# Optimization experiments

Hardware: AMD Instinct MI355X
Metric: run time of the kernel (lower is better)

Reference implementation:

```python
import jax, jax.numpy as jnp
import numpy as np

HEADS = 16
DIM = 1024
SCALE = DIM ** (-0.5)  # scale_with_head=False


def setup_inputs() -> dict:
    key = jax.random.key(0)
    k1, k2, k3, k4, k5 = jax.random.split(key, 5)
    B, N = 8, 1024
    x = jax.random.normal(k1, (B, N, DIM), dtype=jnp.float32)
    mask = jax.random.bernoulli(k2, 0.9, (B, N - 1))  # bool [B, N-1]
    Wqkv = jax.random.normal(k3, (3 * DIM, DIM), dtype=jnp.float32) * 0.02
    Wout = jax.random.normal(k4, (DIM, DIM), dtype=jnp.float32) * 0.02
    bout = jax.random.normal(k5, (DIM,), dtype=jnp.float32) * 0.02
    return {"x": x, "mask": mask, "Wqkv": Wqkv, "Wout": Wout, "bout": bout}


def reference(x, mask, Wqkv, Wout, bout):
    b, n, dim = x.shape
    h = HEADS
    d = dim // h
    qkv = x @ Wqkv.T  # [b, n, 3*dim]
    q, k, v = jnp.split(qkv, 3, axis=-1)
    # b n (h d) -> b h n d
    def to_heads(t):
        return t.reshape(b, n, h, d).transpose(0, 2, 1, 3)
    q, k, v = to_heads(q), to_heads(k), to_heads(v)
    dots = jnp.einsum('bhid,bhjd->bhij', q, k) * SCALE  # [b, h, n, n]
    # F.pad(mask.flatten(1), (1,0), value=True) -> prepend always-true token
    m = jnp.pad(mask, ((0, 0), (1, 0)), constant_values=True)  # [b, n]
    pair = m[:, None, None, :] & m[:, None, :, None]  # [b, 1, n, n]
    mask_value = -jnp.finfo(dots.dtype).max
    dots = jnp.where(pair, dots, mask_value)
    attn = jax.nn.softmax(dots, axis=-1)
    out = jnp.einsum('bhij,bhjd->bhid', attn, v)  # [b, h, n, d]
    out = out.transpose(0, 2, 1, 3).reshape(b, n, dim)  # b h n d -> b n (h d)
    out = out @ Wout.T + bout  # to_out (dropout=0 -> identity)
    return out
```

## Files before the change

### kernel.cpp

```cpp
#include <hip/hip_runtime.h>
#include <hip/hip_bf16.h>
#include <stdint.h>

typedef __hip_bfloat16 bf16;
typedef unsigned short u16;
typedef __attribute__((ext_vector_type(8))) short short8;
typedef __attribute__((ext_vector_type(4))) float f32x4;
typedef __attribute__((ext_vector_type(16))) float f32x16;
typedef __attribute__((ext_vector_type(4))) int int4v;

#define BATCH 8
#define SEQ   1024
#define DIM   1024
#define NHEAD 16
#define HD    64
#define SCALE 0.03125f
#define C2    0.04508422f

static __device__ __forceinline__ f32x4 mfma_bf16(short8 a, short8 b, f32x4 c) {
    return __builtin_amdgcn_mfma_f32_16x16x32_bf16(a, b, c, 0, 0, 0);
}
static __device__ __forceinline__ f32x16 mfma32(short8 a, short8 b, f32x16 c) {
    return __builtin_amdgcn_mfma_f32_32x32x16_bf16(a, b, c, 0, 0, 0);
}
static __device__ __forceinline__ unsigned cvt_pk_bf16(float lo, float hi) {
    unsigned r;
    asm("v_cvt_pk_bf16_f32 %0, %1, %2" : "=v"(r) : "v"(lo), "v"(hi));
    return r;
}
static __device__ __forceinline__ void gload16(const u16* g, u16* l) {
    __builtin_amdgcn_global_load_lds(
        (const __attribute__((address_space(1))) void*)g,
        (__attribute__((address_space(3))) void*)l, 16, 0, 0);
}

static __device__ __forceinline__ void conv_seg(const void* src, u16* dst,
                                                int total, int bloc, int bcnt,
                                                bool f32in)
{
    for (int i = bloc * 256 + (int)threadIdx.x; i < total; i += bcnt * 256) {
        if (f32in) {
            const float4 a = ((const float4*)src)[2 * i];
            const float4 b = ((const float4*)src)[2 * i + 1];
            short8 o;
            o[0] = (short)__builtin_bit_cast(u16, __float2bfloat16(a.x));
            o[1] = (short)__builtin_bit_cast(u16, __float2bfloat16(a.y));
            o[2] = (short)__builtin_bit_cast(u16, __float2bfloat16(a.z));
            o[3] = (short)__builtin_bit_cast(u16, __float2bfloat16(a.w));
            o[4] = (short)__builtin_bit_cast(u16, __float2bfloat16(b.x));
            o[5] = (short)__builtin_bit_cast(u16, __float2bfloat16(b.y));
            o[6] = (short)__builtin_bit_cast(u16, __float2bfloat16(b.z));
            o[7] = (short)__builtin_bit_cast(u16, __float2bfloat16(b.w));
            ((short8*)dst)[i] = o;
        } else {
            ((short8*)dst)[i] = ((const short8*)src)[i];
        }
    }
}

__global__ __launch_bounds__(256)
void prep_all(const void* __restrict__ x, const void* __restrict__ mask,
              const void* __restrict__ wq, const void* __restrict__ wo,
              const void* __restrict__ bo,
              u16* __restrict__ xb, u16* __restrict__ wqb,
              u16* __restrict__ wob, u16* __restrict__ bob,
              unsigned long long* __restrict__ mask64)
{
    __shared__ int s_cnt[2];
    if (threadIdx.x == 0) { s_cnt[0] = 0; s_cnt[1] = 0; }
    __syncthreads();
    {
        const uint32_t wx = ((const uint32_t*)x)[threadIdx.x];
        const int e = (int)((wx >> 7) & 0xFFu);
        if (e >= 96 && e <= 159) atomicAdd(&s_cnt[0], 1);
        const uint32_t wm = ((const uint32_t*)mask)[threadIdx.x];
        if (wm > 1u) atomicAdd(&s_cnt[1], 1);
    }
    __syncthreads();
    const bool f32in = (s_cnt[0] < 192);
    const bool mbyte = (s_cnt[1] > 0);

    const int bid = blockIdx.x;
    if (bid < 2048)       conv_seg(x,  xb,  1048576, bid,        2048, f32in);
    else if (bid < 2816)  conv_seg(wq, wqb, 393216,  bid - 2048,  768, f32in);
    else if (bid < 3072)  conv_seg(wo, wob, 131072,  bid - 2816,  256, f32in);
    else if (bid == 3072) conv_seg(bo, bob, 128,     0,             1, f32in);
    else {
        const int b = bid - 3073;
#pragma unroll
        for (int c = 0; c < 4; ++c) {
            const int i = c * 256 + (int)threadIdx.x;
            int v;
            if (i == 0) v = 1;
            else if (mbyte) v = (int)((const uint8_t*)mask)[b * (SEQ - 1) + i - 1];
            else            v = ((const int*)mask)[b * (SEQ - 1) + i - 1];
            v = v ? 1 : 0;
            const unsigned long long bal = __ballot(v);
            if ((i & 63) == 0) mask64[b * 16 + (i >> 6)] = bal;
        }
    }
}

template<int EPI>
__global__ __launch_bounds__(256)
void gemm_bt(const u16* __restrict__ A, const u16* __restrict__ Bm,
             bf16* __restrict__ o0, bf16* __restrict__ o1, bf16* __restrict__ o2,
             float* __restrict__ fo, const u16* __restrict__ bias)
{
    constexpr int K   = 1024;
    constexpr int NT  = K / 64;
    constexpr int BUF = 256 * 64;
    __shared__ u16 lds[2 * BUF];

    const int tid  = threadIdx.x;
    const int lane = tid & 63;
    const int w    = tid >> 6;
    const int wr   = w >> 1, wc = w & 1;
    const int l15  = lane & 15, l4 = lane >> 4;

    const long atile = (long)blockIdx.x * 128;
    const long btile = (long)blockIdx.y * 128;

    const int rl  = lane >> 3;
    const int gs8 = ((lane & 7) ^ rl) * 8;
    const u16* gp[8];
#pragma unroll
    for (int j = 0; j < 8; ++j) {
        const int g = 8 * w + j;
        const int r = g * 8 + rl;
        gp[j] = (r < 128) ? A  + (atile + r) * (long)K + gs8
                          : Bm + (btile + (r - 128)) * (long)K + gs8;
    }

    const int lx  = l4 ^ (l15 & 3);
    const int b2  = (l15 >> 2) & 1;
    const int sl0 = (b2 * 4 + lx) * 8;
    const int sl1 = (((1 ^ b2) * 4) + lx) * 8;
    const int arow = wr * 64 + l15;
    const int brow = 128 + wc * 64 + l15;

    f32x4 acc[4][4];
    const f32x4 fz = {0.f, 0.f, 0.f, 0.f};
#pragma unroll
    for (int i = 0; i < 4; ++i)
#pragma unroll
        for (int j = 0; j < 4; ++j) acc[i][j] = fz;

#define STG(bufo, kt, j) gload16(gp[j] + (size_t)(kt) * 64, \
                                 &lds[(bufo) + (8 * w + (j)) * 512])

#pragma unroll
    for (int j = 0; j < 8; ++j) STG(0, 0, j);
    asm volatile("s_waitcnt vmcnt(0)" ::: "memory");
    __builtin_amdgcn_s_barrier();
    __builtin_amdgcn_sched_barrier(0);

    int cur = 0;
#pragma unroll 1
    for (int kt = 0; kt < NT; ++kt) {
        const int co = cur * BUF;
        const int no = (cur ^ 1) * BUF;
        short8 bfr[2][4], af0, af1;

#pragma unroll
        for (int nt = 0; nt < 4; ++nt) {
            bfr[0][nt] = *(const short8*)&lds[co + (brow + nt * 16) * 64 + sl0];
            bfr[1][nt] = *(const short8*)&lds[co + (brow + nt * 16) * 64 + sl1];
        }
        af0 = *(const short8*)&lds[co + arow * 64 + sl0];
        af1 = *(const short8*)&lds[co + arow * 64 + sl1];
        if (kt + 1 < NT) {
            STG(no, kt + 1, 0); STG(no, kt + 1, 1);
            STG(no, kt + 1, 2); STG(no, kt + 1, 3);
        }
        asm volatile("s_waitcnt lgkmcnt(0)" ::: "memory");
        __builtin_amdgcn_sched_barrier(0);
        __builtin_amdgcn_s_setprio(1);
#pragma unroll
        for (int nt = 0; nt < 4; ++nt) {
            acc[0][nt] = mfma_bf16(af0, bfr[0][nt], acc[0][nt]);
            acc[0][nt] = mfma_bf16(af1, bfr[1][nt], acc[0][nt]);
        }
        __builtin_amdgcn_s_setprio(0);

#pragma unroll
        for (int mt = 1; mt < 4; ++mt) {
            af0 = *(const short8*)&lds[co + (arow + mt * 16) * 64 + sl0];
            af1 = *(const short8*)&lds[co + (arow + mt * 16) * 64 + sl1];
            if (mt == 1 && kt + 1 < NT) {
                STG(no, kt + 1, 4); STG(no, kt + 1, 5);
                STG(no, kt + 1, 6); STG(no, kt + 1, 7);
            }
            asm volatile("s_waitcnt lgkmcnt(0)" ::: "memory");
            __builtin_amdgcn_sched_barrier(0);
            __builtin_amdgcn_s_setprio(1);
#pragma unroll
            for (int nt = 0; nt < 4; ++nt) {
                acc[mt][nt] = mfma_bf16(af0, bfr[0][nt], acc[mt][nt]);
                acc[mt][nt] = mfma_bf16(af1, bfr[1][nt], acc[mt][nt]);
            }
            __builtin_amdgcn_s_setprio(0);
        }

        asm volatile("s_waitcnt vmcnt(0)" ::: "memory");
        __builtin_amdgcn_s_barrier();
        __builtin_amdgcn_sched_barrier(0);
        cur ^= 1;
    }
#undef STG

    const long ci0 = atile + wr * 64;
    const int  cj0 = (int)btile + wc * 64;
#pragma unroll
    for (int mt = 0; mt < 4; ++mt) {
#pragma unroll
        for (int nt = 0; nt < 4; ++nt) {
            const int j = cj0 + nt * 16 + l15;
#pragma unroll
            for (int r = 0; r < 4; ++r) {
                const long i = ci0 + mt * 16 + l4 * 4 + r;
                float vv = acc[mt][nt][r];
                if (EPI == 0) {
                    const int which = j >> 10;
                    const int h     = (j >> 6) & 15;
                    const int dd    = j & 63;
                    const long b    = i >> 10;
                    const long n    = i & 1023;
                    const long bhh  = b * NHEAD + h;
                    if (which == 0)
                        o0[(bhh * SEQ + n) * HD + dd] = __float2bfloat16(vv * C2);
                    else if (which == 1)
                        o1[(bhh * SEQ + n) * HD + dd] = __float2bfloat16(vv);
                    else
                        o2[(bhh * HD + dd) * SEQ + n] = __float2bfloat16(vv);
                } else {
                    const u16 bw = bias[j];
                    vv += __bfloat162float(__builtin_bit_cast(bf16, bw));
                    fo[i * DIM + j] = vv;
                }
            }
        }
    }
}

__global__ __launch_bounds__(256)
void attn_fwd(const bf16* __restrict__ q, const bf16* __restrict__ k,
              const bf16* __restrict__ vt_g,
              const unsigned long long* __restrict__ mask64,
              bf16* __restrict__ o)
{
    __shared__ u16 kl[2][64 * 72];
    __shared__ u16 vl[2][64 * 72];

    const int tid  = threadIdx.x;
    const int lane = tid & 63;
    const int w    = tid >> 6;
    const int l31  = lane & 31;
    const int hi   = lane >> 5;
    const int bh   = blockIdx.x >> 3;
    const int qt   = blockIdx.x & 7;
    const int b    = bh >> 4;
    const int h    = bh & 15;

    const long base  = (long)bh * SEQ * HD;
    const long vbase = (long)bh * HD * SEQ;

    const int qrow = qt * 128 + w * 32 + l31;
    const int mi   = (int)((mask64[b * 16 + (qrow >> 6)] >> (qrow & 63)) & 1ull);

    short8 qf[4];
#pragma unroll
    for (int s4 = 0; s4 < 4; ++s4)
        qf[s4] = *(const short8*)(q + base + (long)qrow * HD + s4 * 16 + hi * 8);
    if (!mi) {
#pragma unroll
        for (int s4 = 0; s4 < 4; ++s4)
            qf[s4] = __builtin_bit_cast(short8, (int4v){0, 0, 0, 0});
    }

    f32x16 oacc0, oacc1, oaccS, zc;
#pragma unroll
    for (int i = 0; i < 16; ++i)
        { oacc0[i] = 0.f; oacc1[i] = 0.f; oaccS[i] = 0.f; zc[i] = 0.f; }

    const u16 NEGW = __builtin_bit_cast(u16, __float2bfloat16(-1e30f));
    const short8 vfB = __builtin_bit_cast(short8,
        (int4v){(hi == 0 && mi) ? 0x3F80 : 0, 0, 0, 0});
    const short8 vfS = __builtin_bit_cast(short8,
        (int4v){0x3F803F80, 0x3F803F80, 0x3F803F80, 0x3F803F80});

    const int sr = tid >> 2, sc = tid & 3;
    short8 rk0 = *(const short8*)(k + base + (long)sr * HD + sc * 8);
    short8 rk1 = *(const short8*)(k + base + (long)sr * HD + 32 + sc * 8);
    short8 rv0 = *(const short8*)(vt_g + vbase + (long)sr * SEQ + sc * 8);
    short8 rv1 = *(const short8*)(vt_g + vbase + (long)sr * SEQ + 32 + sc * 8);
    *(short8*)&kl[0][sr * 72 + sc * 8]      = rk0;
    *(short8*)&kl[0][sr * 72 + 32 + sc * 8] = rk1;
    *(short8*)&vl[0][sr * 72 + sc * 8]      = rv0;
    *(short8*)&vl[0][sr * 72 + 32 + sc * 8] = rv1;
    __syncthreads();

#pragma unroll 1
    for (int t = 0; t < 16; ++t) {
        const int cb = t & 1;
        if (t < 15) {
            const long kn = base + (long)((t + 1) * 64 + sr) * HD;
            rk0 = *(const short8*)(k + kn + sc * 8);
            rk1 = *(const short8*)(k + kn + 32 + sc * 8);
            const long vn = vbase + (long)sr * SEQ + (t + 1) * 64;
            rv0 = *(const short8*)(vt_g + vn + sc * 8);
            rv1 = *(const short8*)(vt_g + vn + 32 + sc * 8);
        }

        const unsigned long long mk = mask64[b * 16 + t];
        const unsigned bit0 = (unsigned)(mk >> l31) & 1u;
        const unsigned bit1 = (unsigned)(mk >> (32 + l31)) & 1u;
        const short8 paB0 = __builtin_bit_cast(short8,
            (int4v){(hi == 0 && !bit0) ? (int)(unsigned)NEGW : 0, 0, 0, 0});
        const short8 paB1 = __builtin_bit_cast(short8,
            (int4v){(hi == 0 && !bit1) ? (int)(unsigned)NEGW : 0, 0, 0, 0});

        f32x16 s0 = mfma32(paB0, vfB, zc);
        f32x16 s1 = mfma32(paB1, vfB, zc);
#pragma unroll
        for (int s4 = 0; s4 < 4; ++s4) {
            const short8 kf0 = *(const short8*)&kl[cb][l31 * 72 + s4 * 16 + hi * 8];
            const short8 kf1 = *(const short8*)&kl[cb][(32 + l31) * 72 + s4 * 16 + hi * 8];
            s0 = mfma32(kf0, qf[s4], s0);
            s1 = mfma32(kf1, qf[s4], s1);
        }

#pragma unroll
        for (int kt = 0; kt < 2; ++kt) {
            const f32x16* sp = kt ? &s1 : &s0;
#pragma unroll
            for (int ks = 0; ks < 2; ++ks) {
                float p[8];
#pragma unroll
                for (int e = 0; e < 8; ++e)
                    p[e] = __builtin_amdgcn_exp2f((*sp)[8 * ks + e]);
                unsigned w0 = cvt_pk_bf16(p[0], p[1]);
                unsigned w1 = cvt_pk_bf16(p[2], p[3]);
                unsigned w2 = cvt_pk_bf16(p[4], p[5]);
                unsigned w3 = cvt_pk_bf16(p[6], p[7]);
                asm volatile("v_permlane32_swap_b32 %0, %1" : "+v"(w0), "+v"(w2));
                asm volatile("v_permlane32_swap_b32 %0, %1" : "+v"(w1), "+v"(w3));
                const short8 pa = __builtin_bit_cast(short8,
                    (int4v){(int)w0, (int)w1, (int)w2, (int)w3});
                const int koff = kt * 32 + ks * 16 + hi * 8;
                const short8 vf0 = *(const short8*)&vl[cb][l31 * 72 + koff];
                const short8 vf1 = *(const short8*)&vl[cb][(32 + l31) * 72 + koff];
                oacc0 = mfma32(pa, vf0, oacc0);
                oacc1 = mfma32(pa, vf1, oacc1);
                oaccS = mfma32(pa, vfS, oaccS);
            }
        }

        if (t < 15) {
            *(short8*)&kl[cb ^ 1][sr * 72 + sc * 8]      = rk0;
            *(short8*)&kl[cb ^ 1][sr * 72 + 32 + sc * 8] = rk1;
            *(short8*)&vl[cb ^ 1][sr * 72 + sc * 8]      = rv0;
            *(short8*)&vl[cb ^ 1][sr * 72 + 32 + sc * 8] = rv1;
        }
        __syncthreads();
    }

#pragma unroll
    for (int g = 0; g < 4; ++g)
#pragma unroll
        for (int j = 0; j < 4; ++j) {
            const int idx = g * 4 + j;
            const float lv = __builtin_amdgcn_rcpf(oaccS[idx]);
            const int qg = qt * 128 + w * 32 + g * 8 + j + 4 * hi;
            const long oaddr = ((long)(b * SEQ + qg)) * DIM + h * HD;
            o[oaddr + l31]      = __float2bfloat16(oacc0[idx] * lv);
            o[oaddr + 32 + l31] = __float2bfloat16(oacc1[idx] * lv);
        }
}

extern "C" void kernel_launch(void* const* d_in, const int* in_sizes, int n_in,
                              void* d_out, int out_size, void* d_ws, size_t ws_size,
                              hipStream_t stream)
{
    (void)in_sizes; (void)n_in; (void)out_size; (void)ws_size;
    const void* x    = d_in[0];
    const void* mask = d_in[1];
    const void* Wqkv = d_in[2];
    const void* Wout = d_in[3];
    const void* bout = d_in[4];
    float* out = (float*)d_out;

    const size_t nX    = (size_t)BATCH * SEQ * DIM;
    const size_t nWqkv = (size_t)3 * DIM * DIM;
    const size_t nWout = (size_t)DIM * DIM;
    const size_t nBout = DIM;
    const size_t per   = (size_t)BATCH * NHEAD * SEQ * HD;

    char* wp = (char*)d_ws;
    u16* xb    = (u16*)wp;                      wp += nX * 2;
    u16* Wqkvb = (u16*)wp;                      wp += nWqkv * 2;
    u16* Woutb = (u16*)wp;                      wp += nWout * 2;
    u16* boutb = (u16*)wp;                      wp += nBout * 2;
    unsigned long long* m64 = (unsigned long long*)wp; wp += BATCH * 16 * 8;
    u16* qb    = (u16*)wp;                      wp += per * 2;
    u16* kb    = (u16*)wp;                      wp += per * 2;
    u16* vb    = (u16*)wp;                      wp += per * 2;

    prep_all<<<3081, 256, 0, stream>>>(x, mask, Wqkv, Wout, bout,
                                       xb, Wqkvb, Woutb, boutb, m64);

    gemm_bt<0><<<dim3(64, 24), 256, 0, stream>>>(xb, Wqkvb,
        (bf16*)qb, (bf16*)kb, (bf16*)vb, nullptr, nullptr);
    bf16* ab = (bf16*)xb;
    attn_fwd<<<dim3(BATCH * NHEAD * 8), 256, 0, stream>>>(
        (const bf16*)qb, (const bf16*)kb, (const bf16*)vb, m64, ab);
    gemm_bt<1><<<dim3(64, 8), 256, 0, stream>>>((const u16*)ab, Woutb,
        nullptr, nullptr, nullptr, out, boutb);
}
```

Before: 159.8 us.

## Widen GEMM block tile to 128x256 and stream B fragments with prefetch

```diff
diff --git a/kernel.cpp b/kernel.cpp
--- a/kernel.cpp
+++ b/kernel.cpp
@@ -102,14 +102,14 @@
 }
 
 template<int EPI>
-__global__ __launch_bounds__(256)
+__global__ __launch_bounds__(256, 1)
 void gemm_bt(const u16* __restrict__ A, const u16* __restrict__ Bm,
              bf16* __restrict__ o0, bf16* __restrict__ o1, bf16* __restrict__ o2,
              float* __restrict__ fo, const u16* __restrict__ bias)
 {
     constexpr int K   = 1024;
     constexpr int NT  = K / 64;
-    constexpr int BUF = 256 * 64;
+    constexpr int BUF = 384 * 64;
     __shared__ u16 lds[2 * BUF];
 
     const int tid  = threadIdx.x;
@@ -119,14 +119,14 @@
     const int l15  = lane & 15, l4 = lane >> 4;
 
     const long atile = (long)blockIdx.x * 128;
-    const long btile = (long)blockIdx.y * 128;
+    const long btile = (long)blockIdx.y * 256;
 
     const int rl  = lane >> 3;
     const int gs8 = ((lane & 7) ^ rl) * 8;
-    const u16* gp[8];
-#pragma unroll
-    for (int j = 0; j < 8; ++j) {
-        const int g = 8 * w + j;
+    const u16* gp[12];
+#pragma unroll
+    for (int j = 0; j < 12; ++j) {
+        const int g = 12 * w + j;
         const int r = g * 8 + rl;
         gp[j] = (r < 128) ? A  + (atile + r) * (long)K + gs8
                           : Bm + (btile + (r - 128)) * (long)K + gs8;
@@ -136,21 +136,21 @@
     const int b2  = (l15 >> 2) & 1;
     const int sl0 = (b2 * 4 + lx) * 8;
     const int sl1 = (((1 ^ b2) * 4) + lx) * 8;
-    const int arow = wr * 64 + l15;
-    const int brow = 128 + wc * 64 + l15;
-
-    f32x4 acc[4][4];
+    const int ar  = wr * 64 + l15;
+    const int br  = 128 + wc * 128 + l15;
+
+    f32x4 acc[4][8];
     const f32x4 fz = {0.f, 0.f, 0.f, 0.f};
 #pragma unroll
     for (int i = 0; i < 4; ++i)
 #pragma unroll
-        for (int j = 0; j < 4; ++j) acc[i][j] = fz;
+        for (int j = 0; j < 8; ++j) acc[i][j] = fz;
 
 #define STG(bufo, kt, j) gload16(gp[j] + (size_t)(kt) * 64, \
-                                 &lds[(bufo) + (8 * w + (j)) * 512])
-
-#pragma unroll
-    for (int j = 0; j < 8; ++j) STG(0, 0, j);
+                                 &lds[(bufo) + (12 * w + (j)) * 512])
+
+#pragma unroll
+    for (int j = 0; j < 12; ++j) STG(0, 0, j);
     asm volatile("s_waitcnt vmcnt(0)" ::: "memory");
     __builtin_amdgcn_s_barrier();
     __builtin_amdgcn_sched_barrier(0);
@@ -160,46 +160,34 @@
     for (int kt = 0; kt < NT; ++kt) {
         const int co = cur * BUF;
         const int no = (cur ^ 1) * BUF;
-        short8 bfr[2][4], af0, af1;
-
-#pragma unroll
-        for (int nt = 0; nt < 4; ++nt) {
-            bfr[0][nt] = *(const short8*)&lds[co + (brow + nt * 16) * 64 + sl0];
-            bfr[1][nt] = *(const short8*)&lds[co + (brow + nt * 16) * 64 + sl1];
-        }
-        af0 = *(const short8*)&lds[co + arow * 64 + sl0];
-        af1 = *(const short8*)&lds[co + arow * 64 + sl1];
-        if (kt + 1 < NT) {
-            STG(no, kt + 1, 0); STG(no, kt + 1, 1);
-            STG(no, kt + 1, 2); STG(no, kt + 1, 3);
-        }
-        asm volatile("s_waitcnt lgkmcnt(0)" ::: "memory");
-        __builtin_amdgcn_sched_barrier(0);
-        __builtin_amdgcn_s_setprio(1);
-#pragma unroll
-        for (int nt = 0; nt < 4; ++nt) {
-            acc[0][nt] = mfma_bf16(af0, bfr[0][nt], acc[0][nt]);
-            acc[0][nt] = mfma_bf16(af1, bfr[1][nt], acc[0][nt]);
-        }
-        __builtin_amdgcn_s_setprio(0);
-
-#pragma unroll
-        for (int mt = 1; mt < 4; ++mt) {
-            af0 = *(const short8*)&lds[co + (arow + mt * 16) * 64 + sl0];
-            af1 = *(const short8*)&lds[co + (arow + mt * 16) * 64 + sl1];
-            if (mt == 1 && kt + 1 < NT) {
-                STG(no, kt + 1, 4); STG(no, kt + 1, 5);
-                STG(no, kt + 1, 6); STG(no, kt + 1, 7);
+        const bool st = (kt + 1 < NT);
+
+        short8 af[4][2];
+#pragma unroll
+        for (int mt = 0; mt < 4; ++mt) {
+            af[mt][0] = *(const short8*)&lds[co + (ar + mt * 16) * 64 + sl0];
+            af[mt][1] = *(const short8*)&lds[co + (ar + mt * 16) * 64 + sl1];
+        }
+        short8 bc0 = *(const short8*)&lds[co + br * 64 + sl0];
+        short8 bc1 = *(const short8*)&lds[co + br * 64 + sl1];
+
+#pragma unroll
+        for (int p = 0; p < 8; ++p) {
+            short8 bn0, bn1;
+            if (p < 7) {
+                bn0 = *(const short8*)&lds[co + (br + (p + 1) * 16) * 64 + sl0];
+                bn1 = *(const short8*)&lds[co + (br + (p + 1) * 16) * 64 + sl1];
             }
-            asm volatile("s_waitcnt lgkmcnt(0)" ::: "memory");
+            if (p < 6 && st) { STG(no, kt + 1, 2 * p); STG(no, kt + 1, 2 * p + 1); }
+            if (p < 7) asm volatile("s_waitcnt lgkmcnt(2)" ::: "memory");
+            else       asm volatile("s_waitcnt lgkmcnt(0)" ::: "memory");
             __builtin_amdgcn_sched_barrier(0);
-            __builtin_amdgcn_s_setprio(1);
-#pragma unroll
-            for (int nt = 0; nt < 4; ++nt) {
-                acc[mt][nt] = mfma_bf16(af0, bfr[0][nt], acc[mt][nt]);
-                acc[mt][nt] = mfma_bf16(af1, bfr[1][nt], acc[mt][nt]);
-            }
-            __builtin_amdgcn_s_setprio(0);
+#pragma unroll
+            for (int kk = 0; kk < 2; ++kk)
+#pragma unroll
+                for (int mt = 0; mt < 4; ++mt)
+                    acc[mt][p] = mfma_bf16(af[mt][kk], kk ? bc1 : bc0, acc[mt][p]);
+            if (p < 7) { bc0 = bn0; bc1 = bn1; }
         }
 
         asm volatile("s_waitcnt vmcnt(0)" ::: "memory");
@@ -210,11 +198,11 @@
 #undef STG
 
     const long ci0 = atile + wr * 64;
-    const int  cj0 = (int)btile + wc * 64;
+    const int  cj0 = (int)btile + wc * 128;
 #pragma unroll
     for (int mt = 0; mt < 4; ++mt) {
 #pragma unroll
-        for (int nt = 0; nt < 4; ++nt) {
+        for (int nt = 0; nt < 8; ++nt) {
             const int j = cj0 + nt * 16 + l15;
 #pragma unroll
             for (int r = 0; r < 4; ++r) {
@@ -409,11 +397,11 @@
     prep_all<<<3081, 256, 0, stream>>>(x, mask, Wqkv, Wout, bout,
                                        xb, Wqkvb, Woutb, boutb, m64);
 
-    gemm_bt<0><<<dim3(64, 24), 256, 0, stream>>>(xb, Wqkvb,
+    gemm_bt<0><<<dim3(64, 12), 256, 0, stream>>>(xb, Wqkvb,
         (bf16*)qb, (bf16*)kb, (bf16*)vb, nullptr, nullptr);
     bf16* ab = (bf16*)xb;
     attn_fwd<<<dim3(BATCH * NHEAD * 8), 256, 0, stream>>>(
         (const bf16*)qb, (const bf16*)kb, (const bf16*)vb, m64, ab);
-    gemm_bt<1><<<dim3(64, 8), 256, 0, stream>>>((const u16*)ab, Woutb,
+    gemm_bt<1><<<dim3(64, 4), 256, 0, stream>>>((const u16*)ab, Woutb,
         nullptr, nullptr, nullptr, out, boutb);
 }
```

Result: slower. 176.8 us (+10.6%).

## Enlarge GEMM tile to 256x128 with 512 threads and triple-buffered LDS prefetch

Applied to the files above, without the earlier changes.

```diff
diff --git a/kernel.cpp b/kernel.cpp
--- a/kernel.cpp
+++ b/kernel.cpp
@@ -102,15 +102,15 @@
 }
 
 template<int EPI>
-__global__ __launch_bounds__(256)
+__global__ __launch_bounds__(512, 1)
 void gemm_bt(const u16* __restrict__ A, const u16* __restrict__ Bm,
              bf16* __restrict__ o0, bf16* __restrict__ o1, bf16* __restrict__ o2,
              float* __restrict__ fo, const u16* __restrict__ bias)
 {
     constexpr int K   = 1024;
     constexpr int NT  = K / 64;
-    constexpr int BUF = 256 * 64;
-    __shared__ u16 lds[2 * BUF];
+    constexpr int BUF = 384 * 64;
+    __shared__ u16 lds[3 * BUF];
 
     const int tid  = threadIdx.x;
     const int lane = tid & 63;
@@ -118,26 +118,26 @@
     const int wr   = w >> 1, wc = w & 1;
     const int l15  = lane & 15, l4 = lane >> 4;
 
-    const long atile = (long)blockIdx.x * 128;
+    const long atile = (long)blockIdx.x * 256;
     const long btile = (long)blockIdx.y * 128;
 
     const int rl  = lane >> 3;
     const int gs8 = ((lane & 7) ^ rl) * 8;
-    const u16* gp[8];
-#pragma unroll
-    for (int j = 0; j < 8; ++j) {
-        const int g = 8 * w + j;
+    const u16* gp[6];
+#pragma unroll
+    for (int j = 0; j < 6; ++j) {
+        const int g = 6 * w + j;
         const int r = g * 8 + rl;
-        gp[j] = (r < 128) ? A  + (atile + r) * (long)K + gs8
-                          : Bm + (btile + (r - 128)) * (long)K + gs8;
+        gp[j] = (r < 256) ? A  + (atile + r) * (long)K + gs8
+                          : Bm + (btile + (r - 256)) * (long)K + gs8;
     }
 
     const int lx  = l4 ^ (l15 & 3);
     const int b2  = (l15 >> 2) & 1;
     const int sl0 = (b2 * 4 + lx) * 8;
     const int sl1 = (((1 ^ b2) * 4) + lx) * 8;
-    const int arow = wr * 64 + l15;
-    const int brow = 128 + wc * 64 + l15;
+    const int ar  = wr * 64 + l15;
+    const int br  = 256 + wc * 64 + l15;
 
     f32x4 acc[4][4];
     const f32x4 fz = {0.f, 0.f, 0.f, 0.f};
@@ -147,32 +147,31 @@
         for (int j = 0; j < 4; ++j) acc[i][j] = fz;
 
 #define STG(bufo, kt, j) gload16(gp[j] + (size_t)(kt) * 64, \
-                                 &lds[(bufo) + (8 * w + (j)) * 512])
-
-#pragma unroll
-    for (int j = 0; j < 8; ++j) STG(0, 0, j);
-    asm volatile("s_waitcnt vmcnt(0)" ::: "memory");
+                                 &lds[(bufo) + (6 * w + (j)) * 512])
+
+#pragma unroll
+    for (int j = 0; j < 6; ++j) STG(0, 0, j);
+#pragma unroll
+    for (int j = 0; j < 6; ++j) STG(BUF, 1, j);
+    asm volatile("s_waitcnt vmcnt(6)" ::: "memory");
     __builtin_amdgcn_s_barrier();
     __builtin_amdgcn_sched_barrier(0);
 
-    int cur = 0;
 #pragma unroll 1
     for (int kt = 0; kt < NT; ++kt) {
-        const int co = cur * BUF;
-        const int no = (cur ^ 1) * BUF;
+        const int co = (kt % 3) * BUF;
+        const int so = ((kt + 2) % 3) * BUF;
+        const bool st = (kt + 2 < NT);
         short8 bfr[2][4], af0, af1;
 
 #pragma unroll
         for (int nt = 0; nt < 4; ++nt) {
-            bfr[0][nt] = *(const short8*)&lds[co + (brow + nt * 16) * 64 + sl0];
-            bfr[1][nt] = *(const short8*)&lds[co + (brow + nt * 16) * 64 + sl1];
-        }
-        af0 = *(const short8*)&lds[co + arow * 64 + sl0];
-        af1 = *(const short8*)&lds[co + arow * 64 + sl1];
-        if (kt + 1 < NT) {
-            STG(no, kt + 1, 0); STG(no, kt + 1, 1);
-            STG(no, kt + 1, 2); STG(no, kt + 1, 3);
-        }
+            bfr[0][nt] = *(const short8*)&lds[co + (br + nt * 16) * 64 + sl0];
+            bfr[1][nt] = *(const short8*)&lds[co + (br + nt * 16) * 64 + sl1];
+        }
+        af0 = *(const short8*)&lds[co + ar * 64 + sl0];
+        af1 = *(const short8*)&lds[co + ar * 64 + sl1];
+        if (st) { STG(so, kt + 2, 0); STG(so, kt + 2, 1); }
         asm volatile("s_waitcnt lgkmcnt(0)" ::: "memory");
         __builtin_amdgcn_sched_barrier(0);
         __builtin_amdgcn_s_setprio(1);
@@ -185,12 +184,9 @@
 
 #pragma unroll
         for (int mt = 1; mt < 4; ++mt) {
-            af0 = *(const short8*)&lds[co + (arow + mt * 16) * 64 + sl0];
-            af1 = *(const short8*)&lds[co + (arow + mt * 16) * 64 + sl1];
-            if (mt == 1 && kt + 1 < NT) {
-                STG(no, kt + 1, 4); STG(no, kt + 1, 5);
-                STG(no, kt + 1, 6); STG(no, kt + 1, 7);
-            }
+            af0 = *(const short8*)&lds[co + (ar + mt * 16) * 64 + sl0];
+            af1 = *(const short8*)&lds[co + (ar + mt * 16) * 64 + sl1];
+            if (st && mt < 3) { STG(so, kt + 2, 2 * mt); STG(so, kt + 2, 2 * mt + 1); }
             asm volatile("s_waitcnt lgkmcnt(0)" ::: "memory");
             __builtin_amdgcn_sched_barrier(0);
             __builtin_amdgcn_s_setprio(1);
@@ -202,10 +198,10 @@
             __builtin_amdgcn_s_setprio(0);
         }
 
-        asm volatile("s_waitcnt vmcnt(0)" ::: "memory");
+        if (st) asm volatile("s_waitcnt vmcnt(6)" ::: "memory");
+        else    asm volatile("s_waitcnt vmcnt(0)" ::: "memory");
         __builtin_amdgcn_s_barrier();
         __builtin_amdgcn_sched_barrier(0);
-        cur ^= 1;
     }
 #undef STG
 
@@ -409,11 +405,11 @@
     prep_all<<<3081, 256, 0, stream>>>(x, mask, Wqkv, Wout, bout,
                                        xb, Wqkvb, Woutb, boutb, m64);
 
-    gemm_bt<0><<<dim3(64, 24), 256, 0, stream>>>(xb, Wqkvb,
+    gemm_bt<0><<<dim3(32, 24), 512, 0, stream>>>(xb, Wqkvb,
         (bf16*)qb, (bf16*)kb, (bf16*)vb, nullptr, nullptr);
     bf16* ab = (bf16*)xb;
     attn_fwd<<<dim3(BATCH * NHEAD * 8), 256, 0, stream>>>(
         (const bf16*)qb, (const bf16*)kb, (const bf16*)vb, m64, ab);
-    gemm_bt<1><<<dim3(64, 8), 256, 0, stream>>>((const u16*)ab, Woutb,
+    gemm_bt<1><<<dim3(32, 8), 512, 0, stream>>>((const u16*)ab, Woutb,
         nullptr, nullptr, nullptr, out, boutb);
 }
```

Result: slower. 168.2 us (+5.3%).
